# Kernel optimization log

Measured on AMD Instinct MI355X. Metric: run time of the kernel, lower is better.

Reference implementation:

```python
import jax, jax.numpy as jnp
import numpy as np

NUM_GROUP = 16
LN_EPS = 1e-5


def setup_inputs() -> dict:
    key = jax.random.key(0)
    ks = jax.random.split(key, 3)
    B, N, C = 8, 4096, 1024
    x = jax.random.normal(ks[0], (B, N, C), dtype=jnp.float32)
    Wqkv = jax.random.normal(ks[1], (C, 3 * C), dtype=jnp.float32) * (C ** -0.5)
    Wproj = jax.random.normal(ks[2], (C, C), dtype=jnp.float32) * (C ** -0.5)
    bproj = jnp.zeros((C,), dtype=jnp.float32)
    gamma = jnp.ones((C,), dtype=jnp.float32)
    beta = jnp.zeros((C,), dtype=jnp.float32)
    return {"x": x, "Wqkv": Wqkv, "Wproj": Wproj, "bproj": bproj,
            "gamma": gamma, "beta": beta}


def reference(x, Wqkv, Wproj, bproj, gamma, beta):
    B, N, C = x.shape
    G = NUM_GROUP
    hd = C // G
    scale = hd ** -0.5
    # QKV projection: [B,N,3,G,hd]
    qkv = (x @ Wqkv).reshape(B, N, 3, G, hd)
    q = jnp.transpose(qkv[:, :, 0], (0, 2, 1, 3))  # [B,G,N,hd]
    k = jnp.transpose(qkv[:, :, 1], (0, 2, 1, 3)) * scale
    v = jnp.transpose(qkv[:, :, 2], (0, 2, 1, 3))
    # transposed (channel) attention: k^T @ v -> [B,G,hd,hd]
    attn = jnp.einsum('bgnd,bgne->bgde', k, v)
    attn = jax.nn.softmax(attn, axis=-1)
    # (attn @ q^T)^T : out[b,g,n,d] = sum_e attn[b,g,d,e] * q[b,g,n,e]
    out = jnp.einsum('bgde,bgne->bgnd', attn, q)  # [B,G,N,hd]
    out = jnp.transpose(out, (0, 2, 1, 3)).reshape(B, N, C)
    out = out @ Wproj + bproj  # dropout is identity in eval mode
    h = x + out
    # LayerNorm over last dim
    mu = jnp.mean(h, axis=-1, keepdims=True)
    var = jnp.var(h, axis=-1, keepdims=True)
    return gamma * (h - mu) * jax.lax.rsqrt(var + LN_EPS) + beta
```

## Files before the change

kernel.cpp:

```cpp
#include <hip/hip_runtime.h>
#include <cstdint>

typedef __bf16 bf16;
typedef __bf16 bf16x8 __attribute__((ext_vector_type(8)));
typedef float f32x4 __attribute__((ext_vector_type(4)));

#define DEVI __device__ __forceinline__

DEVI float bits2f(uint32_t u){ union{uint32_t u;float f;}x; x.u=u; return x.f; }

DEVI void gload_lds16(const void* g, void* l){
  __builtin_amdgcn_global_load_lds(
    (const __attribute__((address_space(1))) uint32_t*)g,
    (__attribute__((address_space(3))) uint32_t*)l, 16, 0, 0);
}

__global__ __launch_bounds__(256) void k_cast(const float* __restrict__ x, bf16* __restrict__ o, int n){
  int i = (blockIdx.x*256 + threadIdx.x)*8;
  if (i >= n) return;
  float4 a = *(const float4*)(x+i);
  float4 b = *(const float4*)(x+i+4);
  union { bf16 h[8]; uint4 u; } r;
  r.h[0]=(bf16)a.x; r.h[1]=(bf16)a.y; r.h[2]=(bf16)a.z; r.h[3]=(bf16)a.w;
  r.h[4]=(bf16)b.x; r.h[5]=(bf16)b.y; r.h[6]=(bf16)b.z; r.h[7]=(bf16)b.w;
  *(uint4*)(o+i) = r.u;
}

__global__ __launch_bounds__(256) void k_castT(const float* __restrict__ x, bf16* __restrict__ xb,
                                               bf16* __restrict__ xT){
  const int b = blockIdx.z;
  x  += (size_t)b*4194304; xb += (size_t)b*4194304; xT += (size_t)b*4194304;
  const int n0 = blockIdx.y*64, c0 = blockIdx.x*64;
  __shared__ float sF[64][65];
  const int t = threadIdx.x;
  const int lr = t>>4, lc4 = (t&15)*4;
  #pragma unroll
  for (int i=0;i<4;++i){
    int r = lr + i*16;
    float4 v = *(const float4*)(x + (size_t)(n0+r)*1024 + c0 + lc4);
    sF[r][lc4+0]=v.x; sF[r][lc4+1]=v.y; sF[r][lc4+2]=v.z; sF[r][lc4+3]=v.w;
  }
  __syncthreads();
  const int wr = t>>3, wc8 = (t&7)*8;
  #pragma unroll
  for (int i=0;i<2;++i){
    int r = wr + i*32;
    union{ bf16 h[8]; uint4 u; } p;
    #pragma unroll
    for (int j=0;j<8;++j) p.h[j] = (bf16)sF[r][wc8+j];
    *(uint4*)(xb + (size_t)(n0+r)*1024 + c0 + wc8) = p.u;
  }
  #pragma unroll
  for (int i=0;i<2;++i){
    int c = wr + i*32;
    union{ bf16 h[8]; uint4 u; } p;
    #pragma unroll
    for (int j=0;j<8;++j) p.h[j] = (bf16)sF[wc8+j][c];
    *(uint4*)(xT + (size_t)(c0+c)*4096 + n0 + wc8) = p.u;
  }
}

__global__ __launch_bounds__(256) void k_transpose(const float* __restrict__ W, bf16* __restrict__ WT,
                                                   int R, int Ccols){
  __shared__ float tile[32][33];
  int bc = blockIdx.x*32, br = blockIdx.y*32;
  int lc = threadIdx.x & 31, lr = threadIdx.x >> 5;
  #pragma unroll
  for (int i=0;i<4;i++){
    int r = lr + i*8;
    tile[r][lc] = W[(size_t)(br+r)*Ccols + bc + lc];
  }
  __syncthreads();
  #pragma unroll
  for (int i=0;i<4;i++){
    int r = lr + i*8;
    WT[(size_t)(bc+r)*R + br + lc] = (bf16)tile[lc][r];
  }
}

__global__ __launch_bounds__(256) void k_gemm128(
    const bf16* __restrict__ A, const bf16* __restrict__ BT, bf16* __restrict__ C,
    int N, int K, int lda, int ldb,
    size_t As, size_t Bs, size_t Cs)
{
  A += blockIdx.z*As; BT += blockIdx.z*Bs; C += blockIdx.z*Cs;
  __shared__ __align__(16) bf16 sA[128*64];
  __shared__ __align__(16) bf16 sB[128*64];
  const int t = threadIdx.x, w = t>>6, l = t&63;
  const int bm = blockIdx.y*128, bn = blockIdx.x*128;
  const int wr = (w>>1)*64, wc = (w&1)*64;
  f32x4 acc[4][4] = {};
  const int srow = l>>3;
  const int scol = ((l&7) ^ (l>>3))*8;
  const int nk = K>>6;
  for (int kt=0; kt<nk; ++kt) {
    const int k0 = kt*64;
    #pragma unroll
    for (int i=0;i<4;++i){
      int c = w*4+i;
      int row = c*8 + srow;
      gload_lds16(A  + (size_t)(bm+row)*lda + k0 + scol, (char*)sA + c*1024);
      gload_lds16(BT + (size_t)(bn+row)*ldb + k0 + scol, (char*)sB + c*1024);
    }
    __syncthreads();
    #pragma unroll
    for (int kk=0; kk<64; kk+=32) {
      bf16x8 af[4], bfr[4];
      const int xr = ((kk + 8*(l>>4))*2) ^ ((l&7)<<4);
      #pragma unroll
      for (int mf=0;mf<4;++mf){
        int row = wr + mf*16 + (l&15);
        af[mf] = *(const bf16x8*)((const char*)sA + row*128 + xr);
      }
      #pragma unroll
      for (int nf=0;nf<4;++nf){
        int row = wc + nf*16 + (l&15);
        bfr[nf] = *(const bf16x8*)((const char*)sB + row*128 + xr);
      }
      #pragma unroll
      for (int mf=0;mf<4;++mf)
        #pragma unroll
        for (int nf=0;nf<4;++nf)
          acc[mf][nf] = __builtin_amdgcn_mfma_f32_16x16x32_bf16(af[mf], bfr[nf], acc[mf][nf], 0,0,0);
    }
    __syncthreads();
  }
  #pragma unroll
  for (int mf=0;mf<4;++mf)
    #pragma unroll
    for (int nf=0;nf<4;++nf)
      #pragma unroll
      for (int r=0;r<4;++r){
        int row = bm + wr + mf*16 + (l>>4)*4 + r;
        int col = bn + wc + nf*16 + (l&15);
        C[(size_t)row*N + col] = (bf16)acc[mf][nf][r];
      }
}

__global__ __launch_bounds__(256) void k_gramsplit(const bf16* __restrict__ xT, float* __restrict__ Gp){
  const int d = blockIdx.z*288 + blockIdx.y*36 + blockIdx.x;
  const int vt = (d & 7)*72 + (d >> 3);
  const int b = vt/72;
  const int rem = vt - b*72;
  const int half = rem >= 36 ? 1 : 0;
  const int t36o = rem - 36*half;
  int t36 = t36o;
  int i = 0;
  while (t36 >= 8 - i){ t36 -= 8 - i; ++i; }
  const int j = i + t36;
  const bf16* A = xT + (size_t)b*4194304;
  float* P = Gp + ((size_t)((half*8 + b)*36 + t36o))*16384;
  const int bm = i*128, bn = j*128;
  const int kbase = half*2048;

  __shared__ __align__(16) bf16 sA[128*64];
  __shared__ __align__(16) bf16 sB[128*64];
  const int t = threadIdx.x, w = t>>6, l = t&63;
  const int wr = (w>>1)*64, wc = (w&1)*64;
  f32x4 acc[4][4] = {};
  const int srow = l>>3;
  const int scol = ((l&7) ^ (l>>3))*8;
  for (int kt=0; kt<32; ++kt) {
    const int k0 = kbase + kt*64;
    #pragma unroll
    for (int ii=0;ii<4;++ii){
      int c = w*4+ii;
      int row = c*8 + srow;
      gload_lds16(A + (size_t)(bm+row)*4096 + k0 + scol, (char*)sA + c*1024);
      gload_lds16(A + (size_t)(bn+row)*4096 + k0 + scol, (char*)sB + c*1024);
    }
    __syncthreads();
    #pragma unroll
    for (int kk=0; kk<64; kk+=32) {
      bf16x8 af[4], bfr[4];
      const int xr = ((kk + 8*(l>>4))*2) ^ ((l&7)<<4);
      #pragma unroll
      for (int mf=0;mf<4;++mf)
        af[mf] = *(const bf16x8*)((const char*)sA + (wr+mf*16+(l&15))*128 + xr);
      #pragma unroll
      for (int nf=0;nf<4;++nf)
        bfr[nf] = *(const bf16x8*)((const char*)sB + (wc+nf*16+(l&15))*128 + xr);
      #pragma unroll
      for (int mf=0;mf<4;++mf)
        #pragma unroll
        for (int nf=0;nf<4;++nf)
          acc[mf][nf] = __builtin_amdgcn_mfma_f32_16x16x32_bf16(af[mf], bfr[nf], acc[mf][nf], 0,0,0);
    }
    __syncthreads();
  }
  #pragma unroll
  for (int mf=0;mf<4;++mf)
    #pragma unroll
    for (int nf=0;nf<4;++nf)
      #pragma unroll
      for (int r=0;r<4;++r)
        P[(wr + mf*16 + (l>>4)*4 + r)*128 + wc + nf*16 + (l&15)] = acc[mf][nf][r];
}

__global__ __launch_bounds__(256) void k_gramreduce(const float* __restrict__ Gp, bf16* __restrict__ Gram){
  const int b = blockIdx.y;
  const int t36o = blockIdx.x;
  int t36 = t36o;
  int i = 0;
  while (t36 >= 8 - i){ t36 -= 8 - i; ++i; }
  const int j = i + t36;
  const float* P0 = Gp + ((size_t)(b*36) + t36o)*16384;
  const float* P1 = Gp + ((size_t)((8+b)*36) + t36o)*16384;
  bf16* C = Gram + (size_t)b*1048576;
  const int bm = i*128, bn = j*128;
  __shared__ float sT[128][129];
  const int t = threadIdx.x;
  const int rr = t>>4, cc = (t&15)*8;
  #pragma unroll
  for (int ch=0; ch<8; ++ch){
    const int row = ch*16 + rr;
    const int idx = row*128 + cc;
    float4 a0 = *(const float4*)(P0+idx), a1 = *(const float4*)(P0+idx+4);
    float4 b0 = *(const float4*)(P1+idx), b1 = *(const float4*)(P1+idx+4);
    float s[8] = {a0.x+b0.x, a0.y+b0.y, a0.z+b0.z, a0.w+b0.w,
                  a1.x+b1.x, a1.y+b1.y, a1.z+b1.z, a1.w+b1.w};
    union{ bf16 h[8]; uint4 u; } p;
    #pragma unroll
    for (int k=0;k<8;++k) p.h[k] = (bf16)s[k];
    *(uint4*)(C + (size_t)(bm+row)*1024 + bn + cc) = p.u;
    if (i != j){
      #pragma unroll
      for (int k=0;k<8;++k) sT[row][cc+k] = s[k];
    }
  }
  if (i == j) return;
  __syncthreads();
  #pragma unroll
  for (int ch=0; ch<8; ++ch){
    const int c = ch*16 + rr;
    union{ bf16 h[8]; uint4 u; } p;
    #pragma unroll
    for (int k=0;k<8;++k) p.h[k] = (bf16)sT[cc+k][c];
    *(uint4*)(C + (size_t)(bn+c)*1024 + bm + cc) = p.u;
  }
}

__global__ __launch_bounds__(512, 2) void k_gemm256(
    const bf16* __restrict__ A, const bf16* __restrict__ BT, bf16* __restrict__ C,
    int N, int K,
    const float* __restrict__ bias, const bf16* __restrict__ resid,
    size_t As, size_t Bs, size_t Cs, size_t Rs)
{
  A += blockIdx.z*As; BT += blockIdx.z*Bs; C += blockIdx.z*Cs; resid += blockIdx.z*Rs;
  __shared__ __align__(16) bf16 lds[2][2][256*64];
  bf16* bA0 = &lds[0][0][0]; bf16* bB0 = &lds[0][1][0];
  bf16* bA1 = &lds[1][0][0]; bf16* bB1 = &lds[1][1][0];

  const int t = threadIdx.x, w = t>>6, l = t&63;
  const int wm = w>>2, wn = w&3;

  const int nwg = gridDim.x * gridDim.y;
  const int orig = blockIdx.y * gridDim.x + blockIdx.x;
  const int q = nwg >> 3, r = nwg & 7;
  const int xcd = orig & 7, loc = orig >> 3;
  const int swz = (xcd < r ? xcd*(q+1) : r*(q+1) + (xcd-r)*q) + loc;
  const int bx = swz % gridDim.x, by = swz / gridDim.x;
  const int bm = by*256, bn = bx*256;

  const int co0 = (16*(l>>4)) ^ ((l&7)<<4);
  const int co1 = (64 + 16*(l>>4)) ^ ((l&7)<<4);

  auto stageA = [&](const bf16* G, bf16* Ldst, int j, int k0){
    int row = wm*128 + wn*32 + j*8 + (l>>3);
    int col = 8*((l&7) ^ (l>>3));
    gload_lds16(G + (size_t)(bm + row)*K + k0 + col,
                Ldst + (wm*128 + wn*32 + j*8)*64);
  };
  auto stageB = [&](const bf16* G, bf16* Ldst, int j, int k0){
    int row = j*64 + w*8 + (l>>3);
    int col = 8*((l&7) ^ (l>>3));
    gload_lds16(G + (size_t)(bn + row)*K + k0 + col,
                Ldst + (j*64 + w*8)*64);
  };

#define RD_AA(dst, qd, base) {                                                  \
    const int r0 = wm*128 + (qd)*32 + (l&15);                                   \
    dst[0][0] = *(const bf16x8*)((const char*)(base) + (r0   )*128 + co0);      \
    dst[0][1] = *(const bf16x8*)((const char*)(base) + (r0   )*128 + co1);      \
    dst[1][0] = *(const bf16x8*)((const char*)(base) + (r0+16)*128 + co0);      \
    dst[1][1] = *(const bf16x8*)((const char*)(base) + (r0+16)*128 + co1);      \
  }

#define MFMA_Q(P, AA) {                                                         \
    __builtin_amdgcn_s_setprio(1);                                              \
    _Pragma("unroll")                                                           \
    for (int kk=0;kk<2;++kk)                                                    \
      _Pragma("unroll")                                                         \
      for (int i=0;i<2;++i)                                                     \
        _Pragma("unroll")                                                       \
        for (int nf=0;nf<4;++nf)                                                \
          acc[2*(P)+i][nf] = __builtin_amdgcn_mfma_f32_16x16x32_bf16(           \
              AA[i][kk], bfr[nf][kk], acc[2*(P)+i][nf], 0,0,0);                 \
    __builtin_amdgcn_s_setprio(0);                                              \
  }

#define BAR asm volatile("s_barrier" ::: "memory")

  f32x4 acc[8][4] = {};
  const int NT = K >> 6;

  #pragma unroll
  for (int j=0;j<4;++j) stageA(A, bA0, j, 0);
  #pragma unroll
  for (int j=0;j<4;++j) stageB(BT, bB0, j, 0);
  __builtin_amdgcn_sched_barrier(0);
  if (NT > 1){
    #pragma unroll
    for (int j=0;j<4;++j) stageB(BT, bB1, j, 64);
    asm volatile("s_waitcnt vmcnt(4)" ::: "memory");
  } else {
    asm volatile("s_waitcnt vmcnt(0)" ::: "memory");
  }
  BAR;

  bf16x8 aaA[2][2], aaB[2][2];
  RD_AA(aaA, wn, bA0);

  for (int T = 0; T < NT; ++T){
    bf16* sA  = (T&1) ? bA1 : bA0;
    bf16* sB  = (T&1) ? bB1 : bB0;
    bf16* sAn = (T&1) ? bA0 : bA1;
    const int kA = (T+1)<<6, kB = (T+2)<<6;
    const bool stA = (T+1) < NT, stB = (T+2) < NT;

    bf16x8 bfr[4][2];
    const int rb = wn*64 + (l&15);
    #pragma unroll
    for (int nf=0;nf<4;++nf){
      bfr[nf][0] = *(const bf16x8*)((const char*)sB + (rb+nf*16)*128 + co0);
      bfr[nf][1] = *(const bf16x8*)((const char*)sB + (rb+nf*16)*128 + co1);
    }

    RD_AA(aaB, (wn+1)&3, sA);
    if (stA){ stageA(A, sAn, 0, kA); stageA(A, sAn, 1, kA); }
    BAR; MFMA_Q(0, aaA); BAR;

    RD_AA(aaA, (wn+2)&3, sA);
    if (stA){ stageA(A, sAn, 2, kA); stageA(A, sAn, 3, kA); }
    BAR; MFMA_Q(1, aaB); BAR;

    RD_AA(aaB, (wn+3)&3, sA);
    if (stB){ stageB(BT, sB, 0, kB); stageB(BT, sB, 1, kB); }
    BAR; MFMA_Q(2, aaA); BAR;

    if (stB){
      stageB(BT, sB, 2, kB); stageB(BT, sB, 3, kB);
      asm volatile("s_waitcnt vmcnt(4)" ::: "memory");
    } else {
      asm volatile("s_waitcnt vmcnt(0)" ::: "memory");
    }
    if (stA) RD_AA(aaA, wn, sAn);
    BAR; MFMA_Q(3, aaB); BAR;
  }
#undef RD_AA
#undef MFMA_Q
#undef BAR

  #pragma unroll
  for (int P=0; P<4; ++P){
    const int qd = (P+wn)&3;
    #pragma unroll
    for (int i=0;i<2;++i){
      #pragma unroll
      for (int nf=0; nf<4; ++nf){
        #pragma unroll
        for (int r2=0; r2<4; ++r2){
          int row = bm + wm*128 + qd*32 + i*16 + (l>>4)*4 + r2;
          int col = bn + wn*64 + nf*16 + (l&15);
          float v = acc[2*P+i][nf][r2] + bias[col] + (float)resid[(size_t)row*N + col];
          C[(size_t)row*N + col] = (bf16)v;
        }
      }
    }
  }
}

__global__ __launch_bounds__(256) void k_sgemm64(const bf16* __restrict__ T2, const bf16* __restrict__ WqkvT,
                                                 bf16* __restrict__ Aatt){
  const int bg = blockIdx.x, b = bg>>4, g = bg&15;
  const bf16* Arows = T2 + (size_t)b*1048576 + (size_t)(g*64)*1024;
  const bf16* Brows = WqkvT + (size_t)(2048 + g*64)*1024;
  __shared__ __align__(16) bf16 sA[64*64];
  __shared__ __align__(16) bf16 sB[64*64];
  const int t = threadIdx.x, w = t>>6, l = t&63;
  const int srow = l>>3, scol = ((l&7)^(l>>3))*8;
  f32x4 acc[4] = {};
  for (int kt=0; kt<16; ++kt){
    const int k0 = kt*64;
    gload_lds16(Arows + (size_t)(w*8+srow)*1024 + k0 + scol,      sA + (w*8)*64);
    gload_lds16(Arows + (size_t)(32+w*8+srow)*1024 + k0 + scol,   sA + (32+w*8)*64);
    gload_lds16(Brows + (size_t)(w*8+srow)*1024 + k0 + scol,      sB + (w*8)*64);
    gload_lds16(Brows + (size_t)(32+w*8+srow)*1024 + k0 + scol,   sB + (32+w*8)*64);
    __syncthreads();
    #pragma unroll
    for (int kk=0; kk<64; kk+=32){
      const int xr = ((kk + 8*(l>>4))*2) ^ ((l&7)<<4);
      bf16x8 af = *(const bf16x8*)((const char*)sA + (w*16+(l&15))*128 + xr);
      #pragma unroll
      for (int nf=0; nf<4; ++nf){
        bf16x8 bfv = *(const bf16x8*)((const char*)sB + (nf*16+(l&15))*128 + xr);
        acc[nf] = __builtin_amdgcn_mfma_f32_16x16x32_bf16(af, bfv, acc[nf], 0,0,0);
      }
    }
    __syncthreads();
  }
  #pragma unroll
  for (int reg=0; reg<4; ++reg){
    float m = -3.4e38f;
    #pragma unroll
    for (int nf=0; nf<4; ++nf) m = fmaxf(m, acc[nf][reg]);
    m = fmaxf(m, __shfl_xor(m,1)); m = fmaxf(m, __shfl_xor(m,2));
    m = fmaxf(m, __shfl_xor(m,4)); m = fmaxf(m, __shfl_xor(m,8));
    float e[4]; float s = 0.f;
    #pragma unroll
    for (int nf=0; nf<4; ++nf){ e[nf] = __expf((acc[nf][reg]-m)*0.125f); s += e[nf]; }
    s += __shfl_xor(s,1); s += __shfl_xor(s,2); s += __shfl_xor(s,4); s += __shfl_xor(s,8);
    const float inv = 1.0f/s;
    const int row = w*16 + (l>>4)*4 + reg;
    #pragma unroll
    for (int nf=0; nf<4; ++nf)
      Aatt[(size_t)bg*4096 + row*64 + nf*16 + (l&15)] = (bf16)(e[nf]*inv);
  }
}

__global__ __launch_bounds__(256) void k_applyW(const bf16* __restrict__ Wqkvb, const bf16* __restrict__ Aatt,
                                                bf16* __restrict__ U){
  const int bg = blockIdx.y, b = bg>>4, g = bg&15;
  const int m0 = blockIdx.x*128;
  __shared__ __align__(16) bf16 Pl[64][72];
  const int t = threadIdx.x, w = t>>6, l = t&63;
  for (int idx=t; idx<1024; idx+=256){
    int r2 = idx>>4, c4 = (idx&15)*4;
    *(uint2*)&Pl[r2][c4] = *(const uint2*)&Aatt[(size_t)bg*4096 + r2*64 + c4];
  }
  __syncthreads();
  f32x4 acc[2][4] = {};
  const bf16* Ab = Wqkvb + (size_t)(m0 + w*32)*3072 + g*64;
  #pragma unroll
  for (int kk=0; kk<64; kk+=32){
    bf16x8 af[2], pf[4];
    #pragma unroll
    for (int mf=0;mf<2;++mf)
      af[mf] = *(const bf16x8*)(Ab + (size_t)(mf*16 + (l&15))*3072 + kk + 8*(l>>4));
    #pragma unroll
    for (int nf=0;nf<4;++nf)
      pf[nf] = *(const bf16x8*)&Pl[nf*16 + (l&15)][kk + 8*(l>>4)];
    #pragma unroll
    for (int mf=0;mf<2;++mf)
      #pragma unroll
      for (int nf=0;nf<4;++nf)
        acc[mf][nf] = __builtin_amdgcn_mfma_f32_16x16x32_bf16(af[mf], pf[nf], acc[mf][nf], 0,0,0);
  }
  #pragma unroll
  for (int mf=0;mf<2;++mf)
    #pragma unroll
    for (int nf=0;nf<4;++nf)
      #pragma unroll
      for (int r=0;r<4;++r){
        int rowc = m0 + w*32 + mf*16 + (l>>4)*4 + r;
        int col = g*64 + nf*16 + (l&15);
        U[(size_t)b*1048576 + (size_t)rowc*1024 + col] = (bf16)acc[mf][nf][r];
      }
}

__global__ __launch_bounds__(256) void k_ln(const bf16* __restrict__ h, const float* __restrict__ gamma,
                                            const float* __restrict__ beta, float* __restrict__ y){
  const int w = threadIdx.x>>6, l = threadIdx.x&63;
  const size_t row = (size_t)blockIdx.x*4 + w;
  const bf16* hr = h + row*1024 + l*16;
  uint4 p0 = *(const uint4*)hr;
  uint4 p1 = *(const uint4*)(hr+8);
  float v[16];
  const uint32_t* pw = (const uint32_t*)&p0;
  #pragma unroll
  for (int i=0;i<4;++i){ v[2*i] = bits2f(pw[i]<<16); v[2*i+1] = bits2f(pw[i]&0xffff0000u); }
  const uint32_t* pw1 = (const uint32_t*)&p1;
  #pragma unroll
  for (int i=0;i<4;++i){ v[8+2*i] = bits2f(pw1[i]<<16); v[8+2*i+1] = bits2f(pw1[i]&0xffff0000u); }
  float s=0.f, s2=0.f;
  #pragma unroll
  for (int i=0;i<16;++i){ s+=v[i]; s2+=v[i]*v[i]; }
  #pragma unroll
  for (int off=1; off<64; off<<=1){ s += __shfl_xor(s,off); s2 += __shfl_xor(s2,off); }
  float mu = s*(1.0f/1024.0f);
  float var = s2*(1.0f/1024.0f) - mu*mu;
  float rinv = rsqrtf(var + 1e-5f);
  const float* gp = gamma + l*16; const float* bp = beta + l*16;
  float o[16];
  #pragma unroll
  for (int i=0;i<16;++i) o[i] = gp[i]*(v[i]-mu)*rinv + bp[i];
  float* yr = y + row*1024 + l*16;
  #pragma unroll
  for (int i=0;i<4;++i) ((float4*)yr)[i] = *(float4*)&o[4*i];
}

extern "C" void kernel_launch(void* const* d_in, const int* in_sizes, int n_in,
                              void* d_out, int out_size, void* d_ws, size_t ws_size,
                              hipStream_t stream){
  const float* x     = (const float*)d_in[0];
  const float* Wqkv  = (const float*)d_in[1];
  const float* Wproj = (const float*)d_in[2];
  const float* bproj = (const float*)d_in[3];
  const float* gamma = (const float*)d_in[4];
  const float* beta  = (const float*)d_in[5];
  float* y = (float*)d_out;

  char* ws = (char*)d_ws;
  size_t off = 0;
  auto alloc = [&](size_t bytes)->void*{ void* p = ws + off; off += (bytes + 255) & ~(size_t)255; return p; };
  bf16*  xb     = (bf16*) alloc((size_t)32768*1024*2);
  bf16*  xT     = (bf16*) alloc((size_t)8*1024*4096*2);
  bf16*  Wqkvb  = (bf16*) alloc((size_t)1024*3072*2);
  bf16*  WqkvT  = (bf16*) alloc((size_t)3072*1024*2);
  bf16*  WprojT = (bf16*) alloc((size_t)1024*1024*2);
  bf16*  Gram   = (bf16*) alloc((size_t)8*1024*1024*2);
  bf16*  T2     = (bf16*) alloc((size_t)8*1024*1024*2);
  bf16*  Aatt   = (bf16*) alloc((size_t)128*64*64*2);
  bf16*  U      = (bf16*) alloc((size_t)8*1024*1024*2);
  bf16*  WeffT  = (bf16*) alloc((size_t)8*1024*1024*2);
  float* Gpart  = (float*)alloc((size_t)2*8*36*16384*4);
  bf16*  h      = xT;

  const size_t MB1 = 1048576;

  k_castT<<<dim3(16,64,8),256,0,stream>>>(x, xb, xT);
  k_cast<<<1536,256,0,stream>>>(Wqkv, Wqkvb, 3145728);
  k_transpose<<<dim3(96,32),256,0,stream>>>(Wqkv, WqkvT, 1024, 3072);
  k_transpose<<<dim3(32,32),256,0,stream>>>(Wproj, WprojT, 1024, 1024);
  k_gramsplit<<<dim3(36,8,2),256,0,stream>>>(xT, Gpart);
  k_gramreduce<<<dim3(36,8),256,0,stream>>>(Gpart, Gram);
  k_gemm128<<<dim3(8,8,8),256,0,stream>>>(WqkvT + (size_t)1024*1024, Gram, T2, 1024, 1024, 1024, 1024,
                                          0, MB1, MB1);
  k_sgemm64<<<128,256,0,stream>>>(T2, WqkvT, Aatt);
  k_applyW<<<dim3(8,128),256,0,stream>>>(Wqkvb, Aatt, U);
  k_gemm128<<<dim3(8,8,8),256,0,stream>>>(WprojT, U, WeffT, 1024, 1024, 1024, 1024,
                                          0, MB1, MB1);
  k_gemm256<<<dim3(4,16,8),512,0,stream>>>(xb, WeffT, h, 1024, 1024, bproj, xb,
                                           (size_t)4096*1024, MB1, (size_t)4096*1024, (size_t)4096*1024);
  k_ln<<<8192,256,0,stream>>>(h, gamma, beta, y);
}
```

Before: 350.2 us.

## Split-K the per-group score GEMM and move softmax to a separate kernel

The 64x64 score GEMM per (batch, group) now runs as 8 K-slices across 1024 blocks instead of 128 blocks each looping over the full K. Each slice writes fp32 partial sums into the reused Gpart workspace. A new softmax kernel reduces the partials, applies the scale and writes the bf16 probabilities. The gramsplit block-index remapping is also simplified to use the direct grid mapping. The intent is to fill the GPU better for a small GEMM, at the cost of an extra launch and partial-sum traffic.

```diff
diff --git a/kernel.cpp b/kernel.cpp
--- a/kernel.cpp
+++ b/kernel.cpp
@@ -138,12 +138,9 @@
 }
 
 __global__ __launch_bounds__(256) void k_gramsplit(const bf16* __restrict__ xT, float* __restrict__ Gp){
-  const int d = blockIdx.z*288 + blockIdx.y*36 + blockIdx.x;
-  const int vt = (d & 7)*72 + (d >> 3);
-  const int b = vt/72;
-  const int rem = vt - b*72;
-  const int half = rem >= 36 ? 1 : 0;
-  const int t36o = rem - 36*half;
+  const int t36o = blockIdx.x;
+  const int b = blockIdx.y;
+  const int half = blockIdx.z;
   int t36 = t36o;
   int i = 0;
   while (t36 >= 8 - i){ t36 -= 8 - i; ++i; }
@@ -381,8 +378,8 @@
 }
 
 __global__ __launch_bounds__(256) void k_sgemm64(const bf16* __restrict__ T2, const bf16* __restrict__ WqkvT,
-                                                 bf16* __restrict__ Aatt){
-  const int bg = blockIdx.x, b = bg>>4, g = bg&15;
+                                                 float* __restrict__ Sp){
+  const int ks = blockIdx.x, bg = blockIdx.y, b = bg>>4, g = bg&15;
   const bf16* Arows = T2 + (size_t)b*1048576 + (size_t)(g*64)*1024;
   const bf16* Brows = WqkvT + (size_t)(2048 + g*64)*1024;
   __shared__ __align__(16) bf16 sA[64*64];
@@ -390,8 +387,8 @@
   const int t = threadIdx.x, w = t>>6, l = t&63;
   const int srow = l>>3, scol = ((l&7)^(l>>3))*8;
   f32x4 acc[4] = {};
-  for (int kt=0; kt<16; ++kt){
-    const int k0 = kt*64;
+  for (int kt=0; kt<2; ++kt){
+    const int k0 = ks*128 + kt*64;
     gload_lds16(Arows + (size_t)(w*8+srow)*1024 + k0 + scol,      sA + (w*8)*64);
     gload_lds16(Arows + (size_t)(32+w*8+srow)*1024 + k0 + scol,   sA + (32+w*8)*64);
     gload_lds16(Brows + (size_t)(w*8+srow)*1024 + k0 + scol,      sB + (w*8)*64);
@@ -409,23 +406,41 @@
     }
     __syncthreads();
   }
+  float* o = Sp + ((size_t)ks*128 + bg)*4096;
   #pragma unroll
   for (int reg=0; reg<4; ++reg){
-    float m = -3.4e38f;
-    #pragma unroll
-    for (int nf=0; nf<4; ++nf) m = fmaxf(m, acc[nf][reg]);
-    m = fmaxf(m, __shfl_xor(m,1)); m = fmaxf(m, __shfl_xor(m,2));
-    m = fmaxf(m, __shfl_xor(m,4)); m = fmaxf(m, __shfl_xor(m,8));
-    float e[4]; float s = 0.f;
-    #pragma unroll
-    for (int nf=0; nf<4; ++nf){ e[nf] = __expf((acc[nf][reg]-m)*0.125f); s += e[nf]; }
-    s += __shfl_xor(s,1); s += __shfl_xor(s,2); s += __shfl_xor(s,4); s += __shfl_xor(s,8);
-    const float inv = 1.0f/s;
     const int row = w*16 + (l>>4)*4 + reg;
     #pragma unroll
     for (int nf=0; nf<4; ++nf)
-      Aatt[(size_t)bg*4096 + row*64 + nf*16 + (l&15)] = (bf16)(e[nf]*inv);
-  }
+      o[row*64 + nf*16 + (l&15)] = acc[nf][reg];
+  }
+}
+
+__global__ __launch_bounds__(256) void k_softmax(const float* __restrict__ Sp, bf16* __restrict__ P){
+  const int bg = blockIdx.x;
+  __shared__ float S[64][64];
+  const int t = threadIdx.x;
+  for (int idx=t; idx<4096; idx+=256){
+    float s = 0;
+    #pragma unroll
+    for (int ks=0;ks<8;++ks) s += Sp[((size_t)ks*128+bg)*4096 + idx];
+    S[idx>>6][idx&63] = s * 0.125f;
+  }
+  __syncthreads();
+  const int row = t>>2, qd = t&3;
+  float m = -3.4e38f;
+  #pragma unroll
+  for (int j=0;j<16;++j) m = fmaxf(m, S[row][qd*16+j]);
+  m = fmaxf(m, __shfl_xor(m,1));
+  m = fmaxf(m, __shfl_xor(m,2));
+  float e[16]; float sum = 0.f;
+  #pragma unroll
+  for (int j=0;j<16;++j){ e[j] = __expf(S[row][qd*16+j]-m); sum += e[j]; }
+  sum += __shfl_xor(sum,1);
+  sum += __shfl_xor(sum,2);
+  float inv = 1.0f/sum;
+  #pragma unroll
+  for (int j=0;j<16;++j) P[(size_t)bg*4096 + row*64 + qd*16 + j] = (bf16)(e[j]*inv);
 }
 
 __global__ __launch_bounds__(256) void k_applyW(const bf16* __restrict__ Wqkvb, const bf16* __restrict__ Aatt,
@@ -525,6 +540,7 @@
   bf16*  WeffT  = (bf16*) alloc((size_t)8*1024*1024*2);
   float* Gpart  = (float*)alloc((size_t)2*8*36*16384*4);
   bf16*  h      = xT;
+  float* Sp     = Gpart;
 
   const size_t MB1 = 1048576;
 
@@ -536,7 +552,8 @@
   k_gramreduce<<<dim3(36,8),256,0,stream>>>(Gpart, Gram);
   k_gemm128<<<dim3(8,8,8),256,0,stream>>>(WqkvT + (size_t)1024*1024, Gram, T2, 1024, 1024, 1024, 1024,
                                           0, MB1, MB1);
-  k_sgemm64<<<128,256,0,stream>>>(T2, WqkvT, Aatt);
+  k_sgemm64<<<dim3(8,128),256,0,stream>>>(T2, WqkvT, Sp);
+  k_softmax<<<128,256,0,stream>>>(Sp, Aatt);
   k_applyW<<<dim3(8,128),256,0,stream>>>(Wqkvb, Aatt, U);
   k_gemm128<<<dim3(8,8,8),256,0,stream>>>(WprojT, U, WeffT, 1024, 1024, 1024, 1024,
                                           0, MB1, MB1);
```

After: 372.2 us. 6.3% more time.

## Compute Gram matrix with 256x256 pipelined tiles and three-way split-K

Applied to the files above, without the earlier changes.

Replaces the 128x128 upper-triangular Gram split-K kernel (2-way split, 576 blocks) with a 256x256-tile, double-buffered, 512-thread kernel modeled on the main GEMM, using a 3-way K split (240 blocks). A matching reduction sums three fp32 partials per quadrant and writes mirrored bf16 halves. The goal is higher MFMA efficiency and less LDS/global traffic per FLOP, at the cost of more redundant diagonal-tile work and a larger partial buffer. k_gemm128 also gains an optional bias/residual epilogue template that is currently unused.

```diff
diff --git a/kernel.cpp b/kernel.cpp
--- a/kernel.cpp
+++ b/kernel.cpp
@@ -78,12 +78,15 @@
   }
 }
 
+template<int EPI>
 __global__ __launch_bounds__(256) void k_gemm128(
     const bf16* __restrict__ A, const bf16* __restrict__ BT, bf16* __restrict__ C,
     int N, int K, int lda, int ldb,
-    size_t As, size_t Bs, size_t Cs)
+    size_t As, size_t Bs, size_t Cs,
+    const float* __restrict__ bias, const bf16* __restrict__ resid, size_t Rs)
 {
   A += blockIdx.z*As; BT += blockIdx.z*Bs; C += blockIdx.z*Cs;
+  if (EPI==1) resid += blockIdx.z*Rs;
   __shared__ __align__(16) bf16 sA[128*64];
   __shared__ __align__(16) bf16 sB[128*64];
   const int t = threadIdx.x, w = t>>6, l = t&63;
@@ -133,111 +136,10 @@
       for (int r=0;r<4;++r){
         int row = bm + wr + mf*16 + (l>>4)*4 + r;
         int col = bn + wc + nf*16 + (l&15);
-        C[(size_t)row*N + col] = (bf16)acc[mf][nf][r];
+        float v = acc[mf][nf][r];
+        if (EPI==1) v += bias[col] + (float)resid[(size_t)row*N + col];
+        C[(size_t)row*N + col] = (bf16)v;
       }
-}
-
-__global__ __launch_bounds__(256) void k_gramsplit(const bf16* __restrict__ xT, float* __restrict__ Gp){
-  const int d = blockIdx.z*288 + blockIdx.y*36 + blockIdx.x;
-  const int vt = (d & 7)*72 + (d >> 3);
-  const int b = vt/72;
-  const int rem = vt - b*72;
-  const int half = rem >= 36 ? 1 : 0;
-  const int t36o = rem - 36*half;
-  int t36 = t36o;
-  int i = 0;
-  while (t36 >= 8 - i){ t36 -= 8 - i; ++i; }
-  const int j = i + t36;
-  const bf16* A = xT + (size_t)b*4194304;
-  float* P = Gp + ((size_t)((half*8 + b)*36 + t36o))*16384;
-  const int bm = i*128, bn = j*128;
-  const int kbase = half*2048;
-
-  __shared__ __align__(16) bf16 sA[128*64];
-  __shared__ __align__(16) bf16 sB[128*64];
-  const int t = threadIdx.x, w = t>>6, l = t&63;
-  const int wr = (w>>1)*64, wc = (w&1)*64;
-  f32x4 acc[4][4] = {};
-  const int srow = l>>3;
-  const int scol = ((l&7) ^ (l>>3))*8;
-  for (int kt=0; kt<32; ++kt) {
-    const int k0 = kbase + kt*64;
-    #pragma unroll
-    for (int ii=0;ii<4;++ii){
-      int c = w*4+ii;
-      int row = c*8 + srow;
-      gload_lds16(A + (size_t)(bm+row)*4096 + k0 + scol, (char*)sA + c*1024);
-      gload_lds16(A + (size_t)(bn+row)*4096 + k0 + scol, (char*)sB + c*1024);
-    }
-    __syncthreads();
-    #pragma unroll
-    for (int kk=0; kk<64; kk+=32) {
-      bf16x8 af[4], bfr[4];
-      const int xr = ((kk + 8*(l>>4))*2) ^ ((l&7)<<4);
-      #pragma unroll
-      for (int mf=0;mf<4;++mf)
-        af[mf] = *(const bf16x8*)((const char*)sA + (wr+mf*16+(l&15))*128 + xr);
-      #pragma unroll
-      for (int nf=0;nf<4;++nf)
-        bfr[nf] = *(const bf16x8*)((const char*)sB + (wc+nf*16+(l&15))*128 + xr);
-      #pragma unroll
-      for (int mf=0;mf<4;++mf)
-        #pragma unroll
-        for (int nf=0;nf<4;++nf)
-          acc[mf][nf] = __builtin_amdgcn_mfma_f32_16x16x32_bf16(af[mf], bfr[nf], acc[mf][nf], 0,0,0);
-    }
-    __syncthreads();
-  }
-  #pragma unroll
-  for (int mf=0;mf<4;++mf)
-    #pragma unroll
-    for (int nf=0;nf<4;++nf)
-      #pragma unroll
-      for (int r=0;r<4;++r)
-        P[(wr + mf*16 + (l>>4)*4 + r)*128 + wc + nf*16 + (l&15)] = acc[mf][nf][r];
-}
-
-__global__ __launch_bounds__(256) void k_gramreduce(const float* __restrict__ Gp, bf16* __restrict__ Gram){
-  const int b = blockIdx.y;
-  const int t36o = blockIdx.x;
-  int t36 = t36o;
-  int i = 0;
-  while (t36 >= 8 - i){ t36 -= 8 - i; ++i; }
-  const int j = i + t36;
-  const float* P0 = Gp + ((size_t)(b*36) + t36o)*16384;
-  const float* P1 = Gp + ((size_t)((8+b)*36) + t36o)*16384;
-  bf16* C = Gram + (size_t)b*1048576;
-  const int bm = i*128, bn = j*128;
-  __shared__ float sT[128][129];
-  const int t = threadIdx.x;
-  const int rr = t>>4, cc = (t&15)*8;
-  #pragma unroll
-  for (int ch=0; ch<8; ++ch){
-    const int row = ch*16 + rr;
-    const int idx = row*128 + cc;
-    float4 a0 = *(const float4*)(P0+idx), a1 = *(const float4*)(P0+idx+4);
-    float4 b0 = *(const float4*)(P1+idx), b1 = *(const float4*)(P1+idx+4);
-    float s[8] = {a0.x+b0.x, a0.y+b0.y, a0.z+b0.z, a0.w+b0.w,
-                  a1.x+b1.x, a1.y+b1.y, a1.z+b1.z, a1.w+b1.w};
-    union{ bf16 h[8]; uint4 u; } p;
-    #pragma unroll
-    for (int k=0;k<8;++k) p.h[k] = (bf16)s[k];
-    *(uint4*)(C + (size_t)(bm+row)*1024 + bn + cc) = p.u;
-    if (i != j){
-      #pragma unroll
-      for (int k=0;k<8;++k) sT[row][cc+k] = s[k];
-    }
-  }
-  if (i == j) return;
-  __syncthreads();
-  #pragma unroll
-  for (int ch=0; ch<8; ++ch){
-    const int c = ch*16 + rr;
-    union{ bf16 h[8]; uint4 u; } p;
-    #pragma unroll
-    for (int k=0;k<8;++k) p.h[k] = (bf16)sT[cc+k][c];
-    *(uint4*)(C + (size_t)(bn+c)*1024 + bm + cc) = p.u;
-  }
 }
 
 __global__ __launch_bounds__(512, 2) void k_gemm256(
@@ -377,6 +279,184 @@
         }
       }
     }
+  }
+}
+
+__global__ __launch_bounds__(512, 2) void k_gram256(const bf16* __restrict__ xT, float* __restrict__ Gp){
+  const int t10o = blockIdx.x, b = blockIdx.y, z = blockIdx.z;
+  int td = t10o, i = 0;
+  while (td >= 4 - i){ td -= 4 - i; ++i; }
+  const int j = i + td;
+  const int kofs = (z==0) ? 0 : (z==1 ? 22 : 43);
+  const int NT   = (z==0) ? 22 : 21;
+  const bf16* A = xT + (size_t)b*4194304;
+  float* P = Gp + ((size_t)(z*80 + b*10 + t10o))*65536;
+  const int bm = i*256, bn = j*256;
+
+  __shared__ __align__(16) bf16 lds[2][2][256*64];
+  bf16* bA0 = &lds[0][0][0]; bf16* bB0 = &lds[0][1][0];
+  bf16* bA1 = &lds[1][0][0]; bf16* bB1 = &lds[1][1][0];
+
+  const int t = threadIdx.x, w = t>>6, l = t&63;
+  const int wm = w>>2, wn = w&3;
+
+  const int co0 = (16*(l>>4)) ^ ((l&7)<<4);
+  const int co1 = (64 + 16*(l>>4)) ^ ((l&7)<<4);
+
+  auto stageA = [&](bf16* Ldst, int jj, int k0){
+    int row = wm*128 + wn*32 + jj*8 + (l>>3);
+    int col = 8*((l&7) ^ (l>>3));
+    gload_lds16(A + (size_t)(bm + row)*4096 + k0 + col,
+                Ldst + (wm*128 + wn*32 + jj*8)*64);
+  };
+  auto stageB = [&](bf16* Ldst, int jj, int k0){
+    int row = jj*64 + w*8 + (l>>3);
+    int col = 8*((l&7) ^ (l>>3));
+    gload_lds16(A + (size_t)(bn + row)*4096 + k0 + col,
+                Ldst + (jj*64 + w*8)*64);
+  };
+
+#define RD_AA(dst, qd, base) {                                                  \
+    const int r0 = wm*128 + (qd)*32 + (l&15);                                   \
+    dst[0][0] = *(const bf16x8*)((const char*)(base) + (r0   )*128 + co0);      \
+    dst[0][1] = *(const bf16x8*)((const char*)(base) + (r0   )*128 + co1);      \
+    dst[1][0] = *(const bf16x8*)((const char*)(base) + (r0+16)*128 + co0);      \
+    dst[1][1] = *(const bf16x8*)((const char*)(base) + (r0+16)*128 + co1);      \
+  }
+
+#define MFMA_Q(P, AA) {                                                         \
+    __builtin_amdgcn_s_setprio(1);                                              \
+    _Pragma("unroll")                                                           \
+    for (int kk=0;kk<2;++kk)                                                    \
+      _Pragma("unroll")                                                         \
+      for (int i2=0;i2<2;++i2)                                                  \
+        _Pragma("unroll")                                                       \
+        for (int nf=0;nf<4;++nf)                                                \
+          acc[2*(P)+i2][nf] = __builtin_amdgcn_mfma_f32_16x16x32_bf16(          \
+              AA[i2][kk], bfr[nf][kk], acc[2*(P)+i2][nf], 0,0,0);               \
+    __builtin_amdgcn_s_setprio(0);                                              \
+  }
+
+#define BAR asm volatile("s_barrier" ::: "memory")
+
+  f32x4 acc[8][4] = {};
+  const int k0base = kofs*64;
+
+  #pragma unroll
+  for (int jj=0;jj<4;++jj) stageA(bA0, jj, k0base);
+  #pragma unroll
+  for (int jj=0;jj<4;++jj) stageB(bB0, jj, k0base);
+  __builtin_amdgcn_sched_barrier(0);
+  {
+    #pragma unroll
+    for (int jj=0;jj<4;++jj) stageB(bB1, jj, k0base + 64);
+    asm volatile("s_waitcnt vmcnt(4)" ::: "memory");
+  }
+  BAR;
+
+  bf16x8 aaA[2][2], aaB[2][2];
+  RD_AA(aaA, wn, bA0);
+
+  for (int T = 0; T < NT; ++T){
+    bf16* sA  = (T&1) ? bA1 : bA0;
+    bf16* sB  = (T&1) ? bB1 : bB0;
+    bf16* sAn = (T&1) ? bA0 : bA1;
+    const int kA = k0base + ((T+1)<<6), kB = k0base + ((T+2)<<6);
+    const bool stA = (T+1) < NT, stB = (T+2) < NT;
+
+    bf16x8 bfr[4][2];
+    const int rb = wn*64 + (l&15);
+    #pragma unroll
+    for (int nf=0;nf<4;++nf){
+      bfr[nf][0] = *(const bf16x8*)((const char*)sB + (rb+nf*16)*128 + co0);
+      bfr[nf][1] = *(const bf16x8*)((const char*)sB + (rb+nf*16)*128 + co1);
+    }
+
+    RD_AA(aaB, (wn+1)&3, sA);
+    if (stA){ stageA(sAn, 0, kA); stageA(sAn, 1, kA); }
+    BAR; MFMA_Q(0, aaA); BAR;
+
+    RD_AA(aaA, (wn+2)&3, sA);
+    if (stA){ stageA(sAn, 2, kA); stageA(sAn, 3, kA); }
+    BAR; MFMA_Q(1, aaB); BAR;
+
+    RD_AA(aaB, (wn+3)&3, sA);
+    if (stB){ stageB(sB, 0, kB); stageB(sB, 1, kB); }
+    BAR; MFMA_Q(2, aaA); BAR;
+
+    if (stB){
+      stageB(sB, 2, kB); stageB(sB, 3, kB);
+      asm volatile("s_waitcnt vmcnt(4)" ::: "memory");
+    } else {
+      asm volatile("s_waitcnt vmcnt(0)" ::: "memory");
+    }
+    if (stA) RD_AA(aaA, wn, sAn);
+    BAR; MFMA_Q(3, aaB); BAR;
+  }
+#undef RD_AA
+#undef MFMA_Q
+#undef BAR
+
+  #pragma unroll
+  for (int Pq=0; Pq<4; ++Pq){
+    const int qd = (Pq+wn)&3;
+    #pragma unroll
+    for (int i2=0;i2<2;++i2){
+      #pragma unroll
+      for (int nf=0; nf<4; ++nf){
+        #pragma unroll
+        for (int r2=0; r2<4; ++r2){
+          int row = wm*128 + qd*32 + i2*16 + (l>>4)*4 + r2;
+          int col = wn*64 + nf*16 + (l&15);
+          P[row*256 + col] = acc[2*Pq+i2][nf][r2];
+        }
+      }
+    }
+  }
+}
+
+__global__ __launch_bounds__(256) void k_gramred256(const float* __restrict__ Gp, bf16* __restrict__ Gram){
+  const int t10o = blockIdx.x, b = blockIdx.y, q = blockIdx.z;
+  const int qr = q>>1, qc = q&1;
+  int td = t10o, i = 0;
+  while (td >= 4 - i){ td -= 4 - i; ++i; }
+  const int j = i + td;
+  const float* P0 = Gp + ((size_t)(b*10 + t10o))*65536 + qr*128*256 + qc*128;
+  const float* P1 = P0 + (size_t)80*65536;
+  const float* P2 = P1 + (size_t)80*65536;
+  bf16* C = Gram + (size_t)b*1048576;
+  const int bm = i*256 + qr*128, bn = j*256 + qc*128;
+  const bool domirror = !(i==j && qr==qc);
+  __shared__ float sT[128][129];
+  const int t = threadIdx.x;
+  const int rr = t>>4, cc = (t&15)*8;
+  #pragma unroll
+  for (int ch=0; ch<8; ++ch){
+    const int row = ch*16 + rr;
+    const int idx = row*256 + cc;
+    float4 a0 = *(const float4*)(P0+idx), a1 = *(const float4*)(P0+idx+4);
+    float4 b0 = *(const float4*)(P1+idx), b1 = *(const float4*)(P1+idx+4);
+    float4 c0 = *(const float4*)(P2+idx), c1 = *(const float4*)(P2+idx+4);
+    float s[8] = {a0.x+b0.x+c0.x, a0.y+b0.y+c0.y, a0.z+b0.z+c0.z, a0.w+b0.w+c0.w,
+                  a1.x+b1.x+c1.x, a1.y+b1.y+c1.y, a1.z+b1.z+c1.z, a1.w+b1.w+c1.w};
+    union{ bf16 h[8]; uint4 u; } p;
+    #pragma unroll
+    for (int k=0;k<8;++k) p.h[k] = (bf16)s[k];
+    *(uint4*)(C + (size_t)(bm+row)*1024 + bn + cc) = p.u;
+    if (domirror){
+      #pragma unroll
+      for (int k=0;k<8;++k) sT[row][cc+k] = s[k];
+    }
+  }
+  if (!domirror) return;
+  __syncthreads();
+  #pragma unroll
+  for (int ch=0; ch<8; ++ch){
+    const int c = ch*16 + rr;
+    union{ bf16 h[8]; uint4 u; } p;
+    #pragma unroll
+    for (int k=0;k<8;++k) p.h[k] = (bf16)sT[cc+k][c];
+    *(uint4*)(C + (size_t)(bn+c)*1024 + bm + cc) = p.u;
   }
 }
 
@@ -523,24 +603,25 @@
   bf16*  Aatt   = (bf16*) alloc((size_t)128*64*64*2);
   bf16*  U      = (bf16*) alloc((size_t)8*1024*1024*2);
   bf16*  WeffT  = (bf16*) alloc((size_t)8*1024*1024*2);
-  float* Gpart  = (float*)alloc((size_t)2*8*36*16384*4);
+  float* Gp     = (float*)alloc((size_t)3*80*65536*4);
   bf16*  h      = xT;
 
   const size_t MB1 = 1048576;
+  const size_t MB4 = (size_t)4096*1024;
 
   k_castT<<<dim3(16,64,8),256,0,stream>>>(x, xb, xT);
   k_cast<<<1536,256,0,stream>>>(Wqkv, Wqkvb, 3145728);
   k_transpose<<<dim3(96,32),256,0,stream>>>(Wqkv, WqkvT, 1024, 3072);
   k_transpose<<<dim3(32,32),256,0,stream>>>(Wproj, WprojT, 1024, 1024);
-  k_gramsplit<<<dim3(36,8,2),256,0,stream>>>(xT, Gpart);
-  k_gramreduce<<<dim3(36,8),256,0,stream>>>(Gpart, Gram);
-  k_gemm128<<<dim3(8,8,8),256,0,stream>>>(WqkvT + (size_t)1024*1024, Gram, T2, 1024, 1024, 1024, 1024,
-                                          0, MB1, MB1);
+  k_gram256<<<dim3(10,8,3),512,0,stream>>>(xT, Gp);
+  k_gramred256<<<dim3(10,8,4),256,0,stream>>>(Gp, Gram);
+  k_gemm128<0><<<dim3(8,8,8),256,0,stream>>>(WqkvT + (size_t)1024*1024, Gram, T2, 1024, 1024, 1024, 1024,
+                                             0, MB1, MB1, nullptr, nullptr, 0);
   k_sgemm64<<<128,256,0,stream>>>(T2, WqkvT, Aatt);
   k_applyW<<<dim3(8,128),256,0,stream>>>(Wqkvb, Aatt, U);
-  k_gemm128<<<dim3(8,8,8),256,0,stream>>>(WprojT, U, WeffT, 1024, 1024, 1024, 1024,
-                                          0, MB1, MB1);
+  k_gemm128<0><<<dim3(8,8,8),256,0,stream>>>(WprojT, U, WeffT, 1024, 1024, 1024, 1024,
+                                             0, MB1, MB1, nullptr, nullptr, 0);
   k_gemm256<<<dim3(4,16,8),512,0,stream>>>(xb, WeffT, h, 1024, 1024, bproj, xb,
-                                           (size_t)4096*1024, MB1, (size_t)4096*1024, (size_t)4096*1024);
+                                           MB4, MB1, MB4, MB4);
   k_ln<<<8192,256,0,stream>>>(h, gamma, beta, y);
 }
```

New measurement: 330.9 us. 5.5% less time.
